# Performance work log

Hardware: AMD Instinct MI355X
Metric: run time of the kernel (lower is better)

## Reference

```python
import jax, jax.numpy as jnp
import numpy as np

T, B, D = 256, 16, 512          # time, batch, intermediate_dim (GRU is seq-first)
HR = 256                         # router_dim
EXPERT_DIMS = [0, 128, 256, 512]
NUM_TASKS = 4
COST_EXP = 1.0
BN_EPS = 1e-5


def _gru(x, w_ih, w_hh, b_ih, b_hh):
    """PyTorch-semantics GRU over axis 0. x: (T, ..., D) -> (T, ..., H).
    Works batched (T,B,D) or unbatched (N,D) exactly like nn.GRU."""
    H = w_hh.shape[1]
    gi = x @ w_ih.T + b_ih            # (T, ..., 3H) input projections, done once
    h0 = jnp.zeros(x.shape[1:-1] + (H,), x.dtype)

    def step(h, gi_t):
        gh = h @ w_hh.T + b_hh
        i_r, i_z, i_n = jnp.split(gi_t, 3, axis=-1)
        h_r, h_z, h_n = jnp.split(gh, 3, axis=-1)
        r = jax.nn.sigmoid(i_r + h_r)
        z = jax.nn.sigmoid(i_z + h_z)
        n = jnp.tanh(i_n + r * h_n)
        h_new = (1.0 - z) * n + z * h
        return h_new, h_new

    _, ys = jax.lax.scan(step, h0, gi)
    return ys


def setup_inputs() -> dict:
    key = jax.random.key(0)
    ks = iter(jax.random.split(key, 64))

    def p(shape, fan_in):
        return (jax.random.normal(next(ks), shape, jnp.float32) / np.sqrt(fan_in)).astype(jnp.float32)

    inp = {
        'x': jax.random.normal(next(ks), (T, B, D), jnp.float32),
        'task_ids': jax.random.randint(next(ks), (T, B), 0, NUM_TASKS),
        # router params
        'router_w_ih': p((3 * HR, D), D),
        'router_w_hh': p((3 * HR, HR), HR),
        'router_b_ih': jnp.zeros((3 * HR,), jnp.float32),
        'router_b_hh': jnp.zeros((3 * HR,), jnp.float32),
        'router_out_w': p((len(EXPERT_DIMS), HR), HR),
        'router_out_b': jnp.zeros((len(EXPERT_DIMS),), jnp.float32),
    }
    for i, H in enumerate(EXPERT_DIMS):
        if H == 0:
            continue
        inp[f'e{i}_w_ih'] = p((3 * H, D), D)
        inp[f'e{i}_w_hh'] = p((3 * H, H), H)
        inp[f'e{i}_b_ih'] = jnp.zeros((3 * H,), jnp.float32)
        inp[f'e{i}_b_hh'] = jnp.zeros((3 * H,), jnp.float32)
        inp[f'e{i}_bn_g'] = jnp.ones((H,), jnp.float32)
        inp[f'e{i}_bn_b'] = jnp.zeros((H,), jnp.float32)
        inp[f'e{i}_out_w'] = p((D, H), H)
        inp[f'e{i}_out_b'] = jnp.zeros((D,), jnp.float32)
    return inp


def reference(x, task_ids,
              router_w_ih, router_w_hh, router_b_ih, router_b_hh,
              router_out_w, router_out_b,
              e1_w_ih, e1_w_hh, e1_b_ih, e1_b_hh, e1_bn_g, e1_bn_b, e1_out_w, e1_out_b,
              e2_w_ih, e2_w_hh, e2_b_ih, e2_b_hh, e2_bn_g, e2_bn_b, e2_out_w, e2_out_b,
              e3_w_ih, e3_w_hh, e3_b_ih, e3_b_hh, e3_bn_g, e3_bn_b, e3_out_w, e3_out_b):
    E = len(EXPERT_DIMS)
    # ---- router: GRU -> ReLU -> Linear -> softmax ----
    hs = _gru(x, router_w_ih, router_w_hh, router_b_ih, router_b_hh)   # (T,B,HR)
    logits = jax.nn.relu(hs) @ router_out_w.T + router_out_b           # (T,B,E)
    raw = jax.nn.softmax(logits, axis=-1)                              # raw_router_output
    # no dropout configured -> router_output == raw, all experts active

    # ---- task expert usage losses ----
    costs = jnp.asarray([d ** COST_EXP for d in EXPERT_DIMS], logits.dtype)
    eul = jnp.einsum('tbe,e->tb', raw, costs).reshape(-1)
    tflat = task_ids.reshape(-1)
    sums = jax.ops.segment_sum(eul, tflat, num_segments=NUM_TASKS)
    cnts = jax.ops.segment_sum(jnp.ones_like(eul), tflat, num_segments=NUM_TASKS)
    task_losses = sums / cnts                                           # (NUM_TASKS,)

    # ---- experts: each sees the flat (N,D) tokens as ONE unbatched GRU sequence ----
    flat_x = x.reshape(-1, D)                                           # (N,D)
    gates = raw.reshape(-1, E)                                          # (N,E)
    out = gates[:, 0:1] * flat_x                                        # expert 0 = identity

    eps = [(e1_w_ih, e1_w_hh, e1_b_ih, e1_b_hh, e1_bn_g, e1_bn_b, e1_out_w, e1_out_b),
           (e2_w_ih, e2_w_hh, e2_b_ih, e2_b_hh, e2_bn_g, e2_bn_b, e2_out_w, e2_out_b),
           (e3_w_ih, e3_w_hh, e3_b_ih, e3_b_hh, e3_bn_g, e3_bn_b, e3_out_w, e3_out_b)]
    for i, (w_ih, w_hh, b_ih, b_hh, g, b, ow, ob) in enumerate(eps, start=1):
        h = _gru(flat_x, w_ih, w_hh, b_ih, b_hh)                        # (N,H) unbatched seq
        mu = h.mean(0)
        var = ((h - mu) ** 2).mean(0)                                   # biased var (train-mode BN)
        hn = (h - mu) / jnp.sqrt(var + BN_EPS) * g + b
        eo = jax.nn.relu(hn) @ ow.T + ob                                # (N,D)
        out = out + gates[:, i:i + 1] * eo

    final_output = out.reshape(T, B, D)
    return final_output, raw, task_losses
```

## Files before the change

kernel.cpp:

```cpp
#include <hip/hip_runtime.h>
#include <math.h>

constexpr int TT = 256, BB = 16, DD = 512;
constexpr int NTOK = 4096;
constexpr int RTOT = 3456;
constexpr int E1OFF = 768, E2OFF = 1152, E3OFF = 1920;

constexpr size_t OFF_TSUM = 0;
constexpr size_t OFF_TCNT = 16;
constexpr size_t OFF_CNT  = 32;
constexpr size_t ZBYTES   = 64;
constexpr size_t OFF_GI   = 4096;
constexpr size_t OFF_HS   = OFF_GI  + (size_t)NTOK*RTOT*4;
constexpr size_t OFF_HA3  = OFF_HS  + (size_t)NTOK*256*4;
constexpr size_t OFF_HA2  = OFF_HA3 + (size_t)NTOK*512*4;
constexpr size_t OFF_HA1  = OFF_HA2 + (size_t)NTOK*256*4;
constexpr size_t OFF_AP   = OFF_HA1 + (size_t)NTOK*128*4;
constexpr size_t OFF_MU   = OFF_AP  + (size_t)NTOK*896*4;
constexpr size_t OFF_RSTD = OFF_MU  + 896*4;
constexpr size_t POISON_BYTES = (size_t)NTOK*(256+512+256+128)*4;

__device__ __forceinline__ bool is_poison(float v) {
  return __float_as_uint(v) == 0xAAAAAAAAu;
}

__global__ __launch_bounds__(256) void gemm1_kernel(
    const float* __restrict__ X,
    const float* __restrict__ wR, const float* __restrict__ w1,
    const float* __restrict__ w2, const float* __restrict__ w3,
    const float* __restrict__ bR, const float* __restrict__ b1,
    const float* __restrict__ b2, const float* __restrict__ b3,
    float* __restrict__ GI)
{
  __shared__ float At[32*64];
  __shared__ float Bt[32*64];
  const int n0 = blockIdx.x * 64;
  const int r0 = blockIdx.y * 64;
  const float* W; const float* bias; int rs;
  if (r0 < 768)       { W = wR; bias = bR; rs = 0; }
  else if (r0 < 1152) { W = w1; bias = b1; rs = 768; }
  else if (r0 < 1920) { W = w2; bias = b2; rs = 1152; }
  else                { W = w3; bias = b3; rs = 1920; }
  const int lr0 = r0 - rs;
  const int tid = threadIdx.x;
  const int lm = tid & 63, lk4 = tid >> 6;
  const int tx = tid & 15, ty = tid >> 4;
  float acc[4][4];
#pragma unroll
  for (int i = 0; i < 4; ++i)
#pragma unroll
    for (int q = 0; q < 4; ++q) acc[i][q] = 0.f;

  for (int kb = 0; kb < 512; kb += 32) {
    const float4 a0 = *(const float4*)(X + (size_t)(n0+lm)*512 + kb + lk4*8);
    const float4 a1 = *(const float4*)(X + (size_t)(n0+lm)*512 + kb + lk4*8 + 4);
    const float4 c0 = *(const float4*)(W + (size_t)(lr0+lm)*512 + kb + lk4*8);
    const float4 c1 = *(const float4*)(W + (size_t)(lr0+lm)*512 + kb + lk4*8 + 4);
    __syncthreads();
    At[(lk4*8+0)*64+lm]=a0.x; At[(lk4*8+1)*64+lm]=a0.y; At[(lk4*8+2)*64+lm]=a0.z; At[(lk4*8+3)*64+lm]=a0.w;
    At[(lk4*8+4)*64+lm]=a1.x; At[(lk4*8+5)*64+lm]=a1.y; At[(lk4*8+6)*64+lm]=a1.z; At[(lk4*8+7)*64+lm]=a1.w;
    Bt[(lk4*8+0)*64+lm]=c0.x; Bt[(lk4*8+1)*64+lm]=c0.y; Bt[(lk4*8+2)*64+lm]=c0.z; Bt[(lk4*8+3)*64+lm]=c0.w;
    Bt[(lk4*8+4)*64+lm]=c1.x; Bt[(lk4*8+5)*64+lm]=c1.y; Bt[(lk4*8+6)*64+lm]=c1.z; Bt[(lk4*8+7)*64+lm]=c1.w;
    __syncthreads();
#pragma unroll
    for (int k = 0; k < 32; ++k) {
      const float4 av = *(const float4*)&At[k*64 + ty*4];
      const float4 bv = *(const float4*)&Bt[k*64 + tx*4];
      acc[0][0]=fmaf(av.x,bv.x,acc[0][0]); acc[0][1]=fmaf(av.x,bv.y,acc[0][1]); acc[0][2]=fmaf(av.x,bv.z,acc[0][2]); acc[0][3]=fmaf(av.x,bv.w,acc[0][3]);
      acc[1][0]=fmaf(av.y,bv.x,acc[1][0]); acc[1][1]=fmaf(av.y,bv.y,acc[1][1]); acc[1][2]=fmaf(av.y,bv.z,acc[1][2]); acc[1][3]=fmaf(av.y,bv.w,acc[1][3]);
      acc[2][0]=fmaf(av.z,bv.x,acc[2][0]); acc[2][1]=fmaf(av.z,bv.y,acc[2][1]); acc[2][2]=fmaf(av.z,bv.z,acc[2][2]); acc[2][3]=fmaf(av.z,bv.w,acc[2][3]);
      acc[3][0]=fmaf(av.w,bv.x,acc[3][0]); acc[3][1]=fmaf(av.w,bv.y,acc[3][1]); acc[3][2]=fmaf(av.w,bv.z,acc[3][2]); acc[3][3]=fmaf(av.w,bv.w,acc[3][3]);
    }
  }
  const float4 bb = *(const float4*)(bias + lr0 + tx*4);
#pragma unroll
  for (int i = 0; i < 4; ++i) {
    float4 o;
    o.x = acc[i][0] + bb.x; o.y = acc[i][1] + bb.y; o.z = acc[i][2] + bb.z; o.w = acc[i][3] + bb.w;
    *(float4*)(GI + (size_t)(n0+ty*4+i)*RTOT + r0 + tx*4) = o;
  }
}

struct ScanArgs {
  const float* GI;
  const float* rwhh; const float* rbhh; float* hs;
  const float* w1; const float* b1; float* ha1;
  const float* w2; const float* b2; float* ha2;
  const float* w3; const float* b3; float* ha3;
  int* cnt;
};

template<int H, int OPW>
__device__ void expert_scan(const float* __restrict__ GIe, const float* __restrict__ whh,
                            const float* __restrict__ bhh, float* __restrict__ hall,
                            float* __restrict__ sm, int wg)
{
  constexpr int KCN = 512 / OPW;
  constexpr bool SINGLE = (OPW == H);
  const int tid = threadIdx.x;
  const int j = tid / KCN, kc = tid % KCN;
  const int jg = wg * OPW + j;

  float4 wr[8], wz[8], wn[8];
#pragma unroll
  for (int i4 = 0; i4 < 8; ++i4) {
    const int kk = kc * 32 + ((i4 + kc) & 7) * 4;
    wr[i4] = *(const float4*)(whh + (size_t)jg * H + kk);
    wz[i4] = *(const float4*)(whh + (size_t)(H + jg) * H + kk);
    wn[i4] = *(const float4*)(whh + (size_t)(2*H + jg) * H + kk);
  }
  float gbr = 0.f, gbz = 0.f, gbn = 0.f;
  float gr0 = 0.f, gz0 = 0.f, gn0 = 0.f, gr1 = 0.f, gz1 = 0.f, gn1 = 0.f;
  if (kc == 0) {
    gbr = bhh[jg]; gbz = bhh[H + jg]; gbn = bhh[2*H + jg];
    gr0 = GIe[jg]; gz0 = GIe[H + jg]; gn0 = GIe[2*H + jg];
    const float* g1 = GIe + RTOT;
    gr1 = g1[jg]; gz1 = g1[H + jg]; gn1 = g1[2*H + jg];
  }
  if (SINGLE) {
    if (tid < H) sm[tid] = 0.f;
    __syncthreads();
  }
  for (int t = 0; t < NTOK; ++t) {
    float gr2 = 0.f, gz2 = 0.f, gn2 = 0.f;
    if (kc == 0 && t + 2 < NTOK) {
      const float* g = GIe + (size_t)(t + 2) * RTOT;
      gr2 = g[jg]; gz2 = g[H + jg]; gn2 = g[2*H + jg];
    }
    const float* hbuf;
    if (SINGLE) {
      hbuf = sm + (size_t)(t & 1) * H;
    } else {
      float val = 0.f;
      if (tid < H && t > 0) {
        const volatile float* p = (const volatile float*)(hall + (size_t)(t - 1) * H + tid);
        val = *p;
        while (is_poison(val)) val = *p;
      }
      __syncthreads();
      if (tid < H) sm[tid] = val;
      __syncthreads();
      hbuf = sm;
    }
    float pr = 0.f, pz = 0.f, pn = 0.f;
#pragma unroll
    for (int i4 = 0; i4 < 8; ++i4) {
      const float4 h4 = *(const float4*)(hbuf + kc * 32 + ((i4 + kc) & 7) * 4);
      pr = fmaf(wr[i4].x, h4.x, pr); pr = fmaf(wr[i4].y, h4.y, pr);
      pr = fmaf(wr[i4].z, h4.z, pr); pr = fmaf(wr[i4].w, h4.w, pr);
      pz = fmaf(wz[i4].x, h4.x, pz); pz = fmaf(wz[i4].y, h4.y, pz);
      pz = fmaf(wz[i4].z, h4.z, pz); pz = fmaf(wz[i4].w, h4.w, pz);
      pn = fmaf(wn[i4].x, h4.x, pn); pn = fmaf(wn[i4].y, h4.y, pn);
      pn = fmaf(wn[i4].z, h4.z, pn); pn = fmaf(wn[i4].w, h4.w, pn);
    }
#pragma unroll
    for (int off = KCN / 2; off; off >>= 1) {
      pr += __shfl_down(pr, off); pz += __shfl_down(pz, off); pn += __shfl_down(pn, off);
    }
    if (kc == 0) {
      const float hprev = hbuf[jg];
      const float rg = 1.f / (1.f + expf(-(gr0 + gbr + pr)));
      const float zg = 1.f / (1.f + expf(-(gz0 + gbz + pz)));
      const float nn = tanhf(gn0 + rg * (pn + gbn));
      const float hn = (1.f - zg) * nn + zg * hprev;
      if (SINGLE) {
        sm[(size_t)((t + 1) & 1) * H + jg] = hn;
        hall[(size_t)t * H + jg] = hn;
      } else {
        *(volatile float*)(hall + (size_t)t * H + jg) = hn;
      }
    }
    if (SINGLE) __syncthreads();
    gr0 = gr1; gz0 = gz1; gn0 = gn1;
    gr1 = gr2; gz1 = gz2; gn1 = gn2;
  }
}

__device__ void router_scan(const float* __restrict__ GI, const float* __restrict__ whh,
                            const float* __restrict__ bhh, float* __restrict__ hs,
                            float* __restrict__ sm, int wg)
{
  float* hsmB = sm;
  float* pbuf = sm + 16 * 260;
  const int tid = threadIdx.x;
  const int j = tid >> 4, kc = tid & 15;
  const int jg = wg * 32 + j;
  float4 wr4[4], wz4[4], wn4[4];
#pragma unroll
  for (int i4 = 0; i4 < 4; ++i4) {
    const int kk = kc * 16 + ((i4 + kc) & 3) * 4;
    wr4[i4] = *(const float4*)(whh + (size_t)jg * 256 + kk);
    wz4[i4] = *(const float4*)(whh + (size_t)(256 + jg) * 256 + kk);
    wn4[i4] = *(const float4*)(whh + (size_t)(512 + jg) * 256 + kk);
  }
  const int b2 = tid >> 5, j2 = tid & 31;
  const int jg2 = wg * 32 + j2;
  const float gbr = bhh[jg2], gbz = bhh[256 + jg2], gbn = bhh[512 + jg2];
  float gr0, gz0, gn0, gr1, gz1, gn1;
  { const float* g = GI + (size_t)b2 * RTOT;        gr0 = g[jg2]; gz0 = g[256 + jg2]; gn0 = g[512 + jg2]; }
  { const float* g = GI + (size_t)(16 + b2) * RTOT; gr1 = g[jg2]; gz1 = g[256 + jg2]; gn1 = g[512 + jg2]; }
  const int pb = tid >> 5, pk = (tid & 31) * 8;

  for (int t = 0; t < TT; ++t) {
    float gr2 = 0.f, gz2 = 0.f, gn2 = 0.f;
    if (t + 2 < TT) {
      const float* g = GI + (size_t)((t + 2) * 16 + b2) * RTOT;
      gr2 = g[jg2]; gz2 = g[256 + jg2]; gn2 = g[512 + jg2];
    }
    float v[8];
    if (t == 0) {
#pragma unroll
      for (int u = 0; u < 8; ++u) v[u] = 0.f;
    } else {
      const volatile float* q = (const volatile float*)(hs + (size_t)(t - 1) * 4096 + tid * 8);
#pragma unroll
      for (int u = 0; u < 8; ++u) v[u] = q[u];
      bool bad = true;
      while (bad) {
        bad = false;
#pragma unroll
        for (int u = 0; u < 8; ++u)
          if (is_poison(v[u])) { v[u] = q[u]; bad = true; }
      }
    }
    __syncthreads();
    *(float4*)(hsmB + pb * 260 + pk)     = make_float4(v[0], v[1], v[2], v[3]);
    *(float4*)(hsmB + pb * 260 + pk + 4) = make_float4(v[4], v[5], v[6], v[7]);
    __syncthreads();
    float ar[16], az[16], an[16];
#pragma unroll
    for (int b = 0; b < 16; ++b) { ar[b] = 0.f; az[b] = 0.f; an[b] = 0.f; }
#pragma unroll
    for (int i4 = 0; i4 < 4; ++i4) {
      const int col = kc * 16 + ((i4 + kc) & 3) * 4;
#pragma unroll
      for (int b = 0; b < 16; ++b) {
        const float4 h4 = *(const float4*)(hsmB + b * 260 + col);
        ar[b] = fmaf(wr4[i4].x, h4.x, ar[b]); ar[b] = fmaf(wr4[i4].y, h4.y, ar[b]);
        ar[b] = fmaf(wr4[i4].z, h4.z, ar[b]); ar[b] = fmaf(wr4[i4].w, h4.w, ar[b]);
        az[b] = fmaf(wz4[i4].x, h4.x, az[b]); az[b] = fmaf(wz4[i4].y, h4.y, az[b]);
        az[b] = fmaf(wz4[i4].z, h4.z, az[b]); az[b] = fmaf(wz4[i4].w, h4.w, az[b]);
        an[b] = fmaf(wn4[i4].x, h4.x, an[b]); an[b] = fmaf(wn4[i4].y, h4.y, an[b]);
        an[b] = fmaf(wn4[i4].z, h4.z, an[b]); an[b] = fmaf(wn4[i4].w, h4.w, an[b]);
      }
    }
#pragma unroll
    for (int off = 8; off; off >>= 1) {
#pragma unroll
      for (int b = 0; b < 16; ++b) {
        ar[b] += __shfl_down(ar[b], off);
        az[b] += __shfl_down(az[b], off);
        an[b] += __shfl_down(an[b], off);
      }
    }
    if (kc == 0) {
#pragma unroll
      for (int b = 0; b < 16; ++b) {
        pbuf[(b * 32 + j) * 3 + 0] = ar[b];
        pbuf[(b * 32 + j) * 3 + 1] = az[b];
        pbuf[(b * 32 + j) * 3 + 2] = an[b];
      }
    }
    __syncthreads();
    const float pr = pbuf[(b2 * 32 + j2) * 3 + 0];
    const float pz = pbuf[(b2 * 32 + j2) * 3 + 1];
    const float pn = pbuf[(b2 * 32 + j2) * 3 + 2];
    const float hprev = hsmB[b2 * 260 + jg2];
    const float rg = 1.f / (1.f + expf(-(gr0 + gbr + pr)));
    const float zg = 1.f / (1.f + expf(-(gz0 + gbz + pz)));
    const float nn = tanhf(gn0 + rg * (pn + gbn));
    const float hn = (1.f - zg) * nn + zg * hprev;
    *(volatile float*)(hs + (size_t)t * 4096 + b2 * 256 + jg2) = hn;
    gr0 = gr1; gz0 = gz1; gn0 = gn1;
    gr1 = gr2; gz1 = gz2; gn1 = gn2;
  }
}

__global__ __launch_bounds__(512, 1) void scan_kernel(ScanArgs A)
{
  __shared__ float sm[16 * 260 + 1536];
  __shared__ int role_s[2];
  if (threadIdx.x == 0) {
    unsigned x;
    asm volatile("s_getreg_b32 %0, hwreg(HW_REG_XCC_ID)" : "=s"(x));
    const int xcd = (int)(x & 7u);
    role_s[0] = xcd;
    role_s[1] = atomicAdd(A.cnt + xcd, 1);
  }
  __syncthreads();
  const int xcd = role_s[0], r = role_s[1];
  if (xcd == 0)      { if (r < 16) expert_scan<512, 32>(A.GI + E3OFF, A.w3, A.b3, A.ha3, sm, r); }
  else if (xcd == 1) { if (r < 8)  router_scan(A.GI, A.rwhh, A.rbhh, A.hs, sm, r); }
  else if (xcd == 2) { if (r < 4)  expert_scan<256, 64>(A.GI + E2OFF, A.w2, A.b2, A.ha2, sm, r); }
  else if (xcd == 3) { if (r < 1)  expert_scan<128,128>(A.GI + E1OFF, A.w1, A.b1, A.ha1, sm, r); }
}

__global__ __launch_bounds__(256) void router_out_kernel(
    const float* __restrict__ hs, const float* __restrict__ ow, const float* __restrict__ ob,
    const int* __restrict__ tids, float* __restrict__ raw_out,
    float* __restrict__ tsum, float* __restrict__ tcnt)
{
  const int tid = threadIdx.x;
  const int lane = tid & 63, w = tid >> 6;
  const int n = blockIdx.x * 4 + w;
  float s0 = 0.f, s1 = 0.f, s2 = 0.f, s3 = 0.f;
#pragma unroll
  for (int q = 0; q < 4; ++q) {
    const int jj = lane + q * 64;
    float h = hs[(size_t)n * 256 + jj];
    h = h > 0.f ? h : 0.f;
    s0 = fmaf(h, ow[jj], s0);
    s1 = fmaf(h, ow[256 + jj], s1);
    s2 = fmaf(h, ow[512 + jj], s2);
    s3 = fmaf(h, ow[768 + jj], s3);
  }
  for (int off = 32; off; off >>= 1) {
    s0 += __shfl_xor(s0, off); s1 += __shfl_xor(s1, off);
    s2 += __shfl_xor(s2, off); s3 += __shfl_xor(s3, off);
  }
  if (lane == 0) {
    const float l0 = s0 + ob[0], l1 = s1 + ob[1], l2 = s2 + ob[2], l3 = s3 + ob[3];
    const float m = fmaxf(fmaxf(l0, l1), fmaxf(l2, l3));
    const float e0 = expf(l0 - m), e1 = expf(l1 - m), e2 = expf(l2 - m), e3 = expf(l3 - m);
    const float inv = 1.f / (e0 + e1 + e2 + e3);
    float4 rv; rv.x = e0 * inv; rv.y = e1 * inv; rv.z = e2 * inv; rv.w = e3 * inv;
    *(float4*)(raw_out + (size_t)n * 4) = rv;
    const float eul = rv.y * 128.f + rv.z * 256.f + rv.w * 512.f;
    const int tk = tids[n];
    atomicAdd(&tsum[tk], eul);
    atomicAdd(&tcnt[tk], 1.f);
  }
}

__global__ __launch_bounds__(256) void bn_stats_kernel(
    const float* __restrict__ h1, const float* __restrict__ h2, const float* __restrict__ h3,
    float* __restrict__ mu, float* __restrict__ rstd)
{
  const int c = blockIdx.x;
  const float* hp; int He, hc;
  if (c < 128)      { hp = h1; He = 128; hc = c; }
  else if (c < 384) { hp = h2; He = 256; hc = c - 128; }
  else              { hp = h3; He = 512; hc = c - 384; }
  float s = 0.f, s2 = 0.f;
  for (int r = threadIdx.x; r < NTOK; r += 256) {
    const float v = hp[(size_t)r * He + hc];
    s += v; s2 = fmaf(v, v, s2);
  }
  for (int off = 32; off; off >>= 1) { s += __shfl_xor(s, off); s2 += __shfl_xor(s2, off); }
  __shared__ float red[8];
  const int lane = threadIdx.x & 63, w = threadIdx.x >> 6;
  if (lane == 0) { red[w] = s; red[4 + w] = s2; }
  __syncthreads();
  if (threadIdx.x == 0) {
    const float S = red[0] + red[1] + red[2] + red[3];
    const float S2 = red[4] + red[5] + red[6] + red[7];
    const float m = S * (1.f / 4096.f);
    float v = S2 * (1.f / 4096.f) - m * m;
    v = v > 0.f ? v : 0.f;
    mu[c] = m;
    rstd[c] = 1.f / sqrtf(v + 1e-5f);
  }
}

__global__ __launch_bounds__(256) void aprime_kernel(
    const float* __restrict__ h1, const float* __restrict__ h2, const float* __restrict__ h3,
    const float* __restrict__ g1, const float* __restrict__ be1,
    const float* __restrict__ g2, const float* __restrict__ be2,
    const float* __restrict__ g3, const float* __restrict__ be3,
    const float* __restrict__ mu, const float* __restrict__ rstd,
    const float* __restrict__ raw, float* __restrict__ Ap,
    const float* __restrict__ tsum, const float* __restrict__ tcnt, float* __restrict__ tl_out)
{
  if (blockIdx.x == 4096) {
    if (threadIdx.x < 4) tl_out[threadIdx.x] = tsum[threadIdx.x] / tcnt[threadIdx.x];
    return;
  }
  const int n = blockIdx.x;
  for (int c = threadIdx.x; c < 896; c += 256) {
    const float* hp; const float* gg; const float* bb; int He, hc, e;
    if (c < 128)      { hp = h1; gg = g1; bb = be1; He = 128; hc = c;       e = 1; }
    else if (c < 384) { hp = h2; gg = g2; bb = be2; He = 256; hc = c - 128; e = 2; }
    else              { hp = h3; gg = g3; bb = be3; He = 512; hc = c - 384; e = 3; }
    const float h = hp[(size_t)n * He + hc];
    float v = (h - mu[c]) * rstd[c] * gg[hc] + bb[hc];
    v = v > 0.f ? v : 0.f;
    Ap[(size_t)n * 896 + c] = raw[(size_t)n * 4 + e] * v;
  }
}

__global__ __launch_bounds__(256) void out_gemm_kernel(
    const float* __restrict__ Ap,
    const float* __restrict__ ow1, const float* __restrict__ ow2, const float* __restrict__ ow3,
    const float* __restrict__ ob1, const float* __restrict__ ob2, const float* __restrict__ ob3,
    const float* __restrict__ X, const float* __restrict__ raw, float* __restrict__ out)
{
  __shared__ float At[32*64];
  __shared__ float Bt[32*64];
  const int n0 = blockIdx.x * 64;
  const int d0 = blockIdx.y * 64;
  const int tid = threadIdx.x;
  const int lm = tid & 63, lk4 = tid >> 6;
  const int tx = tid & 15, ty = tid >> 4;
  float acc[4][4];
#pragma unroll
  for (int i = 0; i < 4; ++i)
#pragma unroll
    for (int q = 0; q < 4; ++q) acc[i][q] = 0.f;

  for (int kb = 0; kb < 896; kb += 32) {
    const float* W; int He, ko;
    if (kb < 128)      { W = ow1; He = 128; ko = 0; }
    else if (kb < 384) { W = ow2; He = 256; ko = 128; }
    else               { W = ow3; He = 512; ko = 384; }
    const float4 a0 = *(const float4*)(Ap + (size_t)(n0+lm)*896 + kb + lk4*8);
    const float4 a1 = *(const float4*)(Ap + (size_t)(n0+lm)*896 + kb + lk4*8 + 4);
    const float4 c0 = *(const float4*)(W + (size_t)(d0+lm)*He + (kb - ko) + lk4*8);
    const float4 c1 = *(const float4*)(W + (size_t)(d0+lm)*He + (kb - ko) + lk4*8 + 4);
    __syncthreads();
    At[(lk4*8+0)*64+lm]=a0.x; At[(lk4*8+1)*64+lm]=a0.y; At[(lk4*8+2)*64+lm]=a0.z; At[(lk4*8+3)*64+lm]=a0.w;
    At[(lk4*8+4)*64+lm]=a1.x; At[(lk4*8+5)*64+lm]=a1.y; At[(lk4*8+6)*64+lm]=a1.z; At[(lk4*8+7)*64+lm]=a1.w;
    Bt[(lk4*8+0)*64+lm]=c0.x; Bt[(lk4*8+1)*64+lm]=c0.y; Bt[(lk4*8+2)*64+lm]=c0.z; Bt[(lk4*8+3)*64+lm]=c0.w;
    Bt[(lk4*8+4)*64+lm]=c1.x; Bt[(lk4*8+5)*64+lm]=c1.y; Bt[(lk4*8+6)*64+lm]=c1.z; Bt[(lk4*8+7)*64+lm]=c1.w;
    __syncthreads();
#pragma unroll
    for (int k = 0; k < 32; ++k) {
      const float4 av = *(const float4*)&At[k*64 + ty*4];
      const float4 bv = *(const float4*)&Bt[k*64 + tx*4];
      acc[0][0]=fmaf(av.x,bv.x,acc[0][0]); acc[0][1]=fmaf(av.x,bv.y,acc[0][1]); acc[0][2]=fmaf(av.x,bv.z,acc[0][2]); acc[0][3]=fmaf(av.x,bv.w,acc[0][3]);
      acc[1][0]=fmaf(av.y,bv.x,acc[1][0]); acc[1][1]=fmaf(av.y,bv.y,acc[1][1]); acc[1][2]=fmaf(av.y,bv.z,acc[1][2]); acc[1][3]=fmaf(av.y,bv.w,acc[1][3]);
      acc[2][0]=fmaf(av.z,bv.x,acc[2][0]); acc[2][1]=fmaf(av.z,bv.y,acc[2][1]); acc[2][2]=fmaf(av.z,bv.z,acc[2][2]); acc[2][3]=fmaf(av.z,bv.w,acc[2][3]);
      acc[3][0]=fmaf(av.w,bv.x,acc[3][0]); acc[3][1]=fmaf(av.w,bv.y,acc[3][1]); acc[3][2]=fmaf(av.w,bv.z,acc[3][2]); acc[3][3]=fmaf(av.w,bv.w,acc[3][3]);
    }
  }
#pragma unroll
  for (int i = 0; i < 4; ++i) {
    const int n = n0 + ty * 4 + i;
    const float4 g  = *(const float4*)(raw + (size_t)n * 4);
    const float4 xv = *(const float4*)(X + (size_t)n * 512 + d0 + tx * 4);
    const float4 o1 = *(const float4*)(ob1 + d0 + tx * 4);
    const float4 o2 = *(const float4*)(ob2 + d0 + tx * 4);
    const float4 o3 = *(const float4*)(ob3 + d0 + tx * 4);
    float4 o;
    o.x = acc[i][0] + g.x*xv.x + g.y*o1.x + g.z*o2.x + g.w*o3.x;
    o.y = acc[i][1] + g.x*xv.y + g.y*o1.y + g.z*o2.y + g.w*o3.y;
    o.z = acc[i][2] + g.x*xv.z + g.y*o1.z + g.z*o2.z + g.w*o3.z;
    o.w = acc[i][3] + g.x*xv.w + g.y*o1.w + g.z*o2.w + g.w*o3.w;
    *(float4*)(out + (size_t)n * 512 + d0 + tx * 4) = o;
  }
}

extern "C" void kernel_launch(void* const* d_in, const int* in_sizes, int n_in,
                              void* d_out, int out_size, void* d_ws, size_t ws_size,
                              hipStream_t stream) {
  const float* x    = (const float*)d_in[0];
  const int*   tids = (const int*)d_in[1];
  const float* rwih = (const float*)d_in[2];
  const float* rwhh = (const float*)d_in[3];
  const float* rbih = (const float*)d_in[4];
  const float* rbhh = (const float*)d_in[5];
  const float* row  = (const float*)d_in[6];
  const float* rob  = (const float*)d_in[7];
  const float* w1ih = (const float*)d_in[8];
  const float* w1hh = (const float*)d_in[9];
  const float* b1ih = (const float*)d_in[10];
  const float* b1hh = (const float*)d_in[11];
  const float* bn1g = (const float*)d_in[12];
  const float* bn1b = (const float*)d_in[13];
  const float* ow1  = (const float*)d_in[14];
  const float* ob1  = (const float*)d_in[15];
  const float* w2ih = (const float*)d_in[16];
  const float* w2hh = (const float*)d_in[17];
  const float* b2ih = (const float*)d_in[18];
  const float* b2hh = (const float*)d_in[19];
  const float* bn2g = (const float*)d_in[20];
  const float* bn2b = (const float*)d_in[21];
  const float* ow2  = (const float*)d_in[22];
  const float* ob2  = (const float*)d_in[23];
  const float* w3ih = (const float*)d_in[24];
  const float* w3hh = (const float*)d_in[25];
  const float* b3ih = (const float*)d_in[26];
  const float* b3hh = (const float*)d_in[27];
  const float* bn3g = (const float*)d_in[28];
  const float* bn3b = (const float*)d_in[29];
  const float* ow3  = (const float*)d_in[30];
  const float* ob3  = (const float*)d_in[31];

  char* ws = (char*)d_ws;
  float* tsum = (float*)(ws + OFF_TSUM);
  float* tcnt = (float*)(ws + OFF_TCNT);
  int*   cnt  = (int*)(ws + OFF_CNT);
  float* GI   = (float*)(ws + OFF_GI);
  float* hs   = (float*)(ws + OFF_HS);
  float* ha3  = (float*)(ws + OFF_HA3);
  float* ha2  = (float*)(ws + OFF_HA2);
  float* ha1  = (float*)(ws + OFF_HA1);
  float* Ap   = (float*)(ws + OFF_AP);
  float* mu   = (float*)(ws + OFF_MU);
  float* rstd = (float*)(ws + OFF_RSTD);

  float* outp = (float*)d_out;
  float* rawp = outp + (size_t)NTOK * DD;
  float* tlp  = rawp + (size_t)NTOK * 4;

  hipMemsetAsync(ws, 0, ZBYTES, stream);
  hipMemsetAsync(ws + OFF_HS, 0xAA, POISON_BYTES, stream);

  gemm1_kernel<<<dim3(64, 54), 256, 0, stream>>>(x, rwih, w1ih, w2ih, w3ih,
                                                 rbih, b1ih, b2ih, b3ih, GI);

  ScanArgs sa;
  sa.GI = GI; sa.rwhh = rwhh; sa.rbhh = rbhh; sa.hs = hs;
  sa.w1 = w1hh; sa.b1 = b1hh; sa.ha1 = ha1;
  sa.w2 = w2hh; sa.b2 = b2hh; sa.ha2 = ha2;
  sa.w3 = w3hh; sa.b3 = b3hh; sa.ha3 = ha3;
  sa.cnt = cnt;
  scan_kernel<<<dim3(320), dim3(512), 0, stream>>>(sa);

  router_out_kernel<<<dim3(1024), 256, 0, stream>>>(hs, row, rob, tids, rawp, tsum, tcnt);
  bn_stats_kernel<<<dim3(896), 256, 0, stream>>>(ha1, ha2, ha3, mu, rstd);
  aprime_kernel<<<dim3(4097), 256, 0, stream>>>(ha1, ha2, ha3, bn1g, bn1b, bn2g, bn2b,
                                                bn3g, bn3b, mu, rstd, rawp, Ap,
                                                tsum, tcnt, tlp);

  out_gemm_kernel<<<dim3(64, 8), 256, 0, stream>>>(Ap, ow1, ow2, ow3, ob1, ob2, ob3,
                                                   x, rawp, outp);
}
```

Measured before the change: 6.769 ms.

## Double block size of recurrent scan workgroups and double-buffer hidden state

The persistent scan kernel moves from 512 to 1024 threads per block, halving each thread's slice of the recurrent dot product. Both the expert and router scans now double-buffer the hidden state in shared memory, removing one barrier per step, and hand partial sums to a separate set of gate-update threads through a shared buffer. The goal is a shorter critical path per serial timestep. In exchange the block pays an extra shared-memory round trip and a barrier for the reduction handoff, and carries more register pressure with 1024 threads.

After: 10.43 ms. 54.0% more time.

```diff
diff --git a/kernel.cpp b/kernel.cpp
--- a/kernel.cpp
+++ b/kernel.cpp
@@ -95,57 +95,52 @@
                             const float* __restrict__ bhh, float* __restrict__ hall,
                             float* __restrict__ sm, int wg)
 {
-  constexpr int KCN = 512 / OPW;
+  constexpr int KCN = 1024 / OPW;
+  constexpr int CB = KCN * 4;
   constexpr bool SINGLE = (OPW == H);
   const int tid = threadIdx.x;
   const int j = tid / KCN, kc = tid % KCN;
   const int jg = wg * OPW + j;
-
-  float4 wr[8], wz[8], wn[8];
-#pragma unroll
-  for (int i4 = 0; i4 < 8; ++i4) {
-    const int kk = kc * 32 + ((i4 + kc) & 7) * 4;
+  float* pbuf = sm + 2 * H;
+
+  float4 wr[4], wz[4], wn[4];
+#pragma unroll
+  for (int i4 = 0; i4 < 4; ++i4) {
+    const int kk = i4 * CB + kc * 4;
     wr[i4] = *(const float4*)(whh + (size_t)jg * H + kk);
     wz[i4] = *(const float4*)(whh + (size_t)(H + jg) * H + kk);
-    wn[i4] = *(const float4*)(whh + (size_t)(2*H + jg) * H + kk);
+    wn[i4] = *(const float4*)(whh + (size_t)(2 * H + jg) * H + kk);
   }
   float gbr = 0.f, gbz = 0.f, gbn = 0.f;
   float gr0 = 0.f, gz0 = 0.f, gn0 = 0.f, gr1 = 0.f, gz1 = 0.f, gn1 = 0.f;
-  if (kc == 0) {
-    gbr = bhh[jg]; gbz = bhh[H + jg]; gbn = bhh[2*H + jg];
-    gr0 = GIe[jg]; gz0 = GIe[H + jg]; gn0 = GIe[2*H + jg];
+  const int og = wg * OPW + tid;
+  if (tid < OPW) {
+    gbr = bhh[og]; gbz = bhh[H + og]; gbn = bhh[2 * H + og];
+    gr0 = GIe[og]; gz0 = GIe[H + og]; gn0 = GIe[2 * H + og];
     const float* g1 = GIe + RTOT;
-    gr1 = g1[jg]; gz1 = g1[H + jg]; gn1 = g1[2*H + jg];
-  }
-  if (SINGLE) {
-    if (tid < H) sm[tid] = 0.f;
-    __syncthreads();
-  }
+    gr1 = g1[og]; gz1 = g1[H + og]; gn1 = g1[2 * H + og];
+  }
+  if (SINGLE) { if (tid < H) sm[tid] = 0.f; }
+
   for (int t = 0; t < NTOK; ++t) {
-    float gr2 = 0.f, gz2 = 0.f, gn2 = 0.f;
-    if (kc == 0 && t + 2 < NTOK) {
-      const float* g = GIe + (size_t)(t + 2) * RTOT;
-      gr2 = g[jg]; gz2 = g[H + jg]; gn2 = g[2*H + jg];
-    }
-    const float* hbuf;
-    if (SINGLE) {
-      hbuf = sm + (size_t)(t & 1) * H;
-    } else {
-      float val = 0.f;
-      if (tid < H && t > 0) {
-        const volatile float* p = (const volatile float*)(hall + (size_t)(t - 1) * H + tid);
-        val = *p;
-        while (is_poison(val)) val = *p;
-      }
-      __syncthreads();
-      if (tid < H) sm[tid] = val;
-      __syncthreads();
-      hbuf = sm;
-    }
+    float* cur = sm + (size_t)(t & 1) * H;
+    if (!SINGLE && tid < H / 4) {
+      if (t == 0) {
+        *(float4*)(cur + tid * 4) = make_float4(0.f, 0.f, 0.f, 0.f);
+      } else {
+        const volatile float* q = hall + (size_t)(t - 1) * H + tid * 4;
+        float a = q[0], b = q[1], c = q[2], d = q[3];
+        while (is_poison(a) || is_poison(b) || is_poison(c) || is_poison(d)) {
+          a = q[0]; b = q[1]; c = q[2]; d = q[3];
+        }
+        *(float4*)(cur + tid * 4) = make_float4(a, b, c, d);
+      }
+    }
+    __syncthreads();
     float pr = 0.f, pz = 0.f, pn = 0.f;
 #pragma unroll
-    for (int i4 = 0; i4 < 8; ++i4) {
-      const float4 h4 = *(const float4*)(hbuf + kc * 32 + ((i4 + kc) & 7) * 4);
+    for (int i4 = 0; i4 < 4; ++i4) {
+      const float4 h4 = *(const float4*)(cur + i4 * CB + kc * 4);
       pr = fmaf(wr[i4].x, h4.x, pr); pr = fmaf(wr[i4].y, h4.y, pr);
       pr = fmaf(wr[i4].z, h4.z, pr); pr = fmaf(wr[i4].w, h4.w, pr);
       pz = fmaf(wz[i4].x, h4.x, pz); pz = fmaf(wz[i4].y, h4.y, pz);
@@ -157,128 +152,140 @@
     for (int off = KCN / 2; off; off >>= 1) {
       pr += __shfl_down(pr, off); pz += __shfl_down(pz, off); pn += __shfl_down(pn, off);
     }
-    if (kc == 0) {
-      const float hprev = hbuf[jg];
+    if (kc == 0) { pbuf[j * 3 + 0] = pr; pbuf[j * 3 + 1] = pz; pbuf[j * 3 + 2] = pn; }
+    __syncthreads();
+    if (tid < OPW) {
+      float gr2 = 0.f, gz2 = 0.f, gn2 = 0.f;
+      if (t + 2 < NTOK) {
+        const float* g = GIe + (size_t)(t + 2) * RTOT;
+        gr2 = g[og]; gz2 = g[H + og]; gn2 = g[2 * H + og];
+      }
+      const float prr = pbuf[tid * 3 + 0];
+      const float pzz = pbuf[tid * 3 + 1];
+      const float pnn = pbuf[tid * 3 + 2];
+      const float hprev = cur[og];
+      const float rg = 1.f / (1.f + expf(-(gr0 + gbr + prr)));
+      const float zg = 1.f / (1.f + expf(-(gz0 + gbz + pzz)));
+      const float nn = tanhf(gn0 + rg * (pnn + gbn));
+      const float hn = (1.f - zg) * nn + zg * hprev;
+      if (SINGLE) {
+        sm[(size_t)((t + 1) & 1) * H + og] = hn;
+        hall[(size_t)t * H + og] = hn;
+      } else {
+        *(volatile float*)(hall + (size_t)t * H + og) = hn;
+      }
+      gr0 = gr1; gz0 = gz1; gn0 = gn1;
+      gr1 = gr2; gz1 = gz2; gn1 = gn2;
+    }
+  }
+}
+
+__device__ void router_scan(const float* __restrict__ GI, const float* __restrict__ whh,
+                            const float* __restrict__ bhh, float* __restrict__ hs,
+                            float* __restrict__ sm, int wg)
+{
+  constexpr int RS = 272;
+  float* pbuf = sm + 2 * 16 * RS;
+  const int tid = threadIdx.x;
+  const int j = tid >> 5;
+  const int r5 = tid & 31;
+  const int kc = r5 >> 1;
+  const int bh = r5 & 1;
+  const int jg = wg * 32 + j;
+  float4 wr4[4], wz4[4], wn4[4];
+#pragma unroll
+  for (int i4 = 0; i4 < 4; ++i4) {
+    const int kk = i4 * 64 + kc * 4;
+    wr4[i4] = *(const float4*)(whh + (size_t)jg * 256 + kk);
+    wz4[i4] = *(const float4*)(whh + (size_t)(256 + jg) * 256 + kk);
+    wn4[i4] = *(const float4*)(whh + (size_t)(512 + jg) * 256 + kk);
+  }
+  const int b2 = tid >> 5, j2 = tid & 31;
+  const int jg2 = wg * 32 + j2;
+  float gbr = 0.f, gbz = 0.f, gbn = 0.f;
+  float gr0 = 0.f, gz0 = 0.f, gn0 = 0.f, gr1 = 0.f, gz1 = 0.f, gn1 = 0.f;
+  if (tid < 512) {
+    gbr = bhh[jg2]; gbz = bhh[256 + jg2]; gbn = bhh[512 + jg2];
+    { const float* g = GI + (size_t)b2 * RTOT;        gr0 = g[jg2]; gz0 = g[256 + jg2]; gn0 = g[512 + jg2]; }
+    { const float* g = GI + (size_t)(16 + b2) * RTOT; gr1 = g[jg2]; gz1 = g[256 + jg2]; gn1 = g[512 + jg2]; }
+  }
+  const int sg = tid * 4, sb = sg >> 8, sk = sg & 255;
+
+  for (int t = 0; t < TT; ++t) {
+    float* cur = sm + (size_t)(t & 1) * (16 * RS);
+    {
+      float a, b, c, d;
+      if (t == 0) { a = b = c = d = 0.f; }
+      else {
+        const volatile float* q = hs + (size_t)(t - 1) * 4096 + sg;
+        a = q[0]; b = q[1]; c = q[2]; d = q[3];
+        while (is_poison(a) || is_poison(b) || is_poison(c) || is_poison(d)) {
+          a = q[0]; b = q[1]; c = q[2]; d = q[3];
+        }
+      }
+      *(float4*)(cur + sb * RS + sk) = make_float4(a, b, c, d);
+    }
+    __syncthreads();
+    float ar[8], az[8], an[8];
+#pragma unroll
+    for (int bi = 0; bi < 8; ++bi) { ar[bi] = 0.f; az[bi] = 0.f; an[bi] = 0.f; }
+#pragma unroll
+    for (int i4 = 0; i4 < 4; ++i4) {
+      const int col = i4 * 64 + kc * 4;
+#pragma unroll
+      for (int bi = 0; bi < 8; ++bi) {
+        const float4 h4 = *(const float4*)(cur + (bh * 8 + bi) * RS + col);
+        ar[bi] = fmaf(wr4[i4].x, h4.x, ar[bi]); ar[bi] = fmaf(wr4[i4].y, h4.y, ar[bi]);
+        ar[bi] = fmaf(wr4[i4].z, h4.z, ar[bi]); ar[bi] = fmaf(wr4[i4].w, h4.w, ar[bi]);
+        az[bi] = fmaf(wz4[i4].x, h4.x, az[bi]); az[bi] = fmaf(wz4[i4].y, h4.y, az[bi]);
+        az[bi] = fmaf(wz4[i4].z, h4.z, az[bi]); az[bi] = fmaf(wz4[i4].w, h4.w, az[bi]);
+        an[bi] = fmaf(wn4[i4].x, h4.x, an[bi]); an[bi] = fmaf(wn4[i4].y, h4.y, an[bi]);
+        an[bi] = fmaf(wn4[i4].z, h4.z, an[bi]); an[bi] = fmaf(wn4[i4].w, h4.w, an[bi]);
+      }
+    }
+#pragma unroll
+    for (int off = 16; off >= 2; off >>= 1) {
+#pragma unroll
+      for (int bi = 0; bi < 8; ++bi) {
+        ar[bi] += __shfl_down(ar[bi], off);
+        az[bi] += __shfl_down(az[bi], off);
+        an[bi] += __shfl_down(an[bi], off);
+      }
+    }
+    if (r5 < 2) {
+#pragma unroll
+      for (int bi = 0; bi < 8; ++bi) {
+        const int b = bh * 8 + bi;
+        pbuf[(b * 32 + j) * 3 + 0] = ar[bi];
+        pbuf[(b * 32 + j) * 3 + 1] = az[bi];
+        pbuf[(b * 32 + j) * 3 + 2] = an[bi];
+      }
+    }
+    __syncthreads();
+    if (tid < 512) {
+      float gr2 = 0.f, gz2 = 0.f, gn2 = 0.f;
+      if (t + 2 < TT) {
+        const float* g = GI + (size_t)((t + 2) * 16 + b2) * RTOT;
+        gr2 = g[jg2]; gz2 = g[256 + jg2]; gn2 = g[512 + jg2];
+      }
+      const float pr = pbuf[(b2 * 32 + j2) * 3 + 0];
+      const float pz = pbuf[(b2 * 32 + j2) * 3 + 1];
+      const float pn = pbuf[(b2 * 32 + j2) * 3 + 2];
+      const float hprev = cur[b2 * RS + jg2];
       const float rg = 1.f / (1.f + expf(-(gr0 + gbr + pr)));
       const float zg = 1.f / (1.f + expf(-(gz0 + gbz + pz)));
       const float nn = tanhf(gn0 + rg * (pn + gbn));
       const float hn = (1.f - zg) * nn + zg * hprev;
-      if (SINGLE) {
-        sm[(size_t)((t + 1) & 1) * H + jg] = hn;
-        hall[(size_t)t * H + jg] = hn;
-      } else {
-        *(volatile float*)(hall + (size_t)t * H + jg) = hn;
-      }
-    }
-    if (SINGLE) __syncthreads();
-    gr0 = gr1; gz0 = gz1; gn0 = gn1;
-    gr1 = gr2; gz1 = gz2; gn1 = gn2;
-  }
-}
-
-__device__ void router_scan(const float* __restrict__ GI, const float* __restrict__ whh,
-                            const float* __restrict__ bhh, float* __restrict__ hs,
-                            float* __restrict__ sm, int wg)
-{
-  float* hsmB = sm;
-  float* pbuf = sm + 16 * 260;
-  const int tid = threadIdx.x;
-  const int j = tid >> 4, kc = tid & 15;
-  const int jg = wg * 32 + j;
-  float4 wr4[4], wz4[4], wn4[4];
-#pragma unroll
-  for (int i4 = 0; i4 < 4; ++i4) {
-    const int kk = kc * 16 + ((i4 + kc) & 3) * 4;
-    wr4[i4] = *(const float4*)(whh + (size_t)jg * 256 + kk);
-    wz4[i4] = *(const float4*)(whh + (size_t)(256 + jg) * 256 + kk);
-    wn4[i4] = *(const float4*)(whh + (size_t)(512 + jg) * 256 + kk);
-  }
-  const int b2 = tid >> 5, j2 = tid & 31;
-  const int jg2 = wg * 32 + j2;
-  const float gbr = bhh[jg2], gbz = bhh[256 + jg2], gbn = bhh[512 + jg2];
-  float gr0, gz0, gn0, gr1, gz1, gn1;
-  { const float* g = GI + (size_t)b2 * RTOT;        gr0 = g[jg2]; gz0 = g[256 + jg2]; gn0 = g[512 + jg2]; }
-  { const float* g = GI + (size_t)(16 + b2) * RTOT; gr1 = g[jg2]; gz1 = g[256 + jg2]; gn1 = g[512 + jg2]; }
-  const int pb = tid >> 5, pk = (tid & 31) * 8;
-
-  for (int t = 0; t < TT; ++t) {
-    float gr2 = 0.f, gz2 = 0.f, gn2 = 0.f;
-    if (t + 2 < TT) {
-      const float* g = GI + (size_t)((t + 2) * 16 + b2) * RTOT;
-      gr2 = g[jg2]; gz2 = g[256 + jg2]; gn2 = g[512 + jg2];
-    }
-    float v[8];
-    if (t == 0) {
-#pragma unroll
-      for (int u = 0; u < 8; ++u) v[u] = 0.f;
-    } else {
-      const volatile float* q = (const volatile float*)(hs + (size_t)(t - 1) * 4096 + tid * 8);
-#pragma unroll
-      for (int u = 0; u < 8; ++u) v[u] = q[u];
-      bool bad = true;
-      while (bad) {
-        bad = false;
-#pragma unroll
-        for (int u = 0; u < 8; ++u)
-          if (is_poison(v[u])) { v[u] = q[u]; bad = true; }
-      }
-    }
-    __syncthreads();
-    *(float4*)(hsmB + pb * 260 + pk)     = make_float4(v[0], v[1], v[2], v[3]);
-    *(float4*)(hsmB + pb * 260 + pk + 4) = make_float4(v[4], v[5], v[6], v[7]);
-    __syncthreads();
-    float ar[16], az[16], an[16];
-#pragma unroll
-    for (int b = 0; b < 16; ++b) { ar[b] = 0.f; az[b] = 0.f; an[b] = 0.f; }
-#pragma unroll
-    for (int i4 = 0; i4 < 4; ++i4) {
-      const int col = kc * 16 + ((i4 + kc) & 3) * 4;
-#pragma unroll
-      for (int b = 0; b < 16; ++b) {
-        const float4 h4 = *(const float4*)(hsmB + b * 260 + col);
-        ar[b] = fmaf(wr4[i4].x, h4.x, ar[b]); ar[b] = fmaf(wr4[i4].y, h4.y, ar[b]);
-        ar[b] = fmaf(wr4[i4].z, h4.z, ar[b]); ar[b] = fmaf(wr4[i4].w, h4.w, ar[b]);
-        az[b] = fmaf(wz4[i4].x, h4.x, az[b]); az[b] = fmaf(wz4[i4].y, h4.y, az[b]);
-        az[b] = fmaf(wz4[i4].z, h4.z, az[b]); az[b] = fmaf(wz4[i4].w, h4.w, az[b]);
-        an[b] = fmaf(wn4[i4].x, h4.x, an[b]); an[b] = fmaf(wn4[i4].y, h4.y, an[b]);
-        an[b] = fmaf(wn4[i4].z, h4.z, an[b]); an[b] = fmaf(wn4[i4].w, h4.w, an[b]);
-      }
-    }
-#pragma unroll
-    for (int off = 8; off; off >>= 1) {
-#pragma unroll
-      for (int b = 0; b < 16; ++b) {
-        ar[b] += __shfl_down(ar[b], off);
-        az[b] += __shfl_down(az[b], off);
-        an[b] += __shfl_down(an[b], off);
-      }
-    }
-    if (kc == 0) {
-#pragma unroll
-      for (int b = 0; b < 16; ++b) {
-        pbuf[(b * 32 + j) * 3 + 0] = ar[b];
-        pbuf[(b * 32 + j) * 3 + 1] = az[b];
-        pbuf[(b * 32 + j) * 3 + 2] = an[b];
-      }
-    }
-    __syncthreads();
-    const float pr = pbuf[(b2 * 32 + j2) * 3 + 0];
-    const float pz = pbuf[(b2 * 32 + j2) * 3 + 1];
-    const float pn = pbuf[(b2 * 32 + j2) * 3 + 2];
-    const float hprev = hsmB[b2 * 260 + jg2];
-    const float rg = 1.f / (1.f + expf(-(gr0 + gbr + pr)));
-    const float zg = 1.f / (1.f + expf(-(gz0 + gbz + pz)));
-    const float nn = tanhf(gn0 + rg * (pn + gbn));
-    const float hn = (1.f - zg) * nn + zg * hprev;
-    *(volatile float*)(hs + (size_t)t * 4096 + b2 * 256 + jg2) = hn;
-    gr0 = gr1; gz0 = gz1; gn0 = gn1;
-    gr1 = gr2; gz1 = gz2; gn1 = gn2;
-  }
-}
-
-__global__ __launch_bounds__(512, 1) void scan_kernel(ScanArgs A)
-{
-  __shared__ float sm[16 * 260 + 1536];
+      *(volatile float*)(hs + (size_t)t * 4096 + b2 * 256 + jg2) = hn;
+      gr0 = gr1; gz0 = gz1; gn0 = gn1;
+      gr1 = gr2; gz1 = gz2; gn1 = gn2;
+    }
+  }
+}
+
+__global__ __launch_bounds__(1024, 1) void scan_kernel(ScanArgs A)
+{
+  __shared__ float sm[2 * 16 * 272 + 1536];
   __shared__ int role_s[2];
   if (threadIdx.x == 0) {
     unsigned x;
@@ -292,7 +299,7 @@
   if (xcd == 0)      { if (r < 16) expert_scan<512, 32>(A.GI + E3OFF, A.w3, A.b3, A.ha3, sm, r); }
   else if (xcd == 1) { if (r < 8)  router_scan(A.GI, A.rwhh, A.rbhh, A.hs, sm, r); }
   else if (xcd == 2) { if (r < 4)  expert_scan<256, 64>(A.GI + E2OFF, A.w2, A.b2, A.ha2, sm, r); }
-  else if (xcd == 3) { if (r < 1)  expert_scan<128,128>(A.GI + E1OFF, A.w1, A.b1, A.ha1, sm, r); }
+  else if (xcd == 3) { if (r < 1)  expert_scan<128, 128>(A.GI + E1OFF, A.w1, A.b1, A.ha1, sm, r); }
 }
 
 __global__ __launch_bounds__(256) void router_out_kernel(
@@ -514,7 +521,7 @@
   sa.w2 = w2hh; sa.b2 = b2hh; sa.ha2 = ha2;
   sa.w3 = w3hh; sa.b3 = b3hh; sa.ha3 = ha3;
   sa.cnt = cnt;
-  scan_kernel<<<dim3(320), dim3(512), 0, stream>>>(sa);
+  scan_kernel<<<dim3(320), dim3(1024), 0, stream>>>(sa);
 
   router_out_kernel<<<dim3(1024), 256, 0, stream>>>(hs, row, rob, tids, rawp, tsum, tcnt);
   bn_stats_kernel<<<dim3(896), 256, 0, stream>>>(ha1, ha2, ha3, mu, rstd);
```
